# Optimization experiments

Hardware: AMD Instinct MI355X
Metric: run time of the kernel (lower is better)

## Reference

```python
import jax, jax.numpy as jnp
import numpy as np

# ---- static config ----
B, D, H, W, C = 4, 8, 56, 56, 192
Md, Mh, Mw = 2, 7, 7
Sd, Sh, Sw = 1, 3, 3
NH = 6
HD = C // NH
SCALE = HD ** -0.5
N = Md * Mh * Mw  # 98
NW = (D // Md) * (H // Mh) * (W // Mw)  # 256 windows per batch element


def _rel_pos_index():
    coords = np.stack(np.meshgrid(np.arange(Md), np.arange(Mh), np.arange(Mw), indexing='ij'))
    cf = coords.reshape(3, -1)
    rc = (cf[:, :, None] - cf[:, None, :]).transpose(1, 2, 0)
    rc[..., 0] += Md - 1
    rc[..., 1] += Mh - 1
    rc[..., 2] += Mw - 1
    rc[..., 0] *= (2 * Mh - 1) * (2 * Mw - 1)
    rc[..., 1] *= 2 * Mw - 1
    return rc.sum(-1)  # (N, N) int

REL_IDX = jnp.asarray(_rel_pos_index())


def _build_attn_mask():
    img = np.zeros((D, H, W), dtype=np.float32)
    cnt = 0
    for ds in (slice(0, -Md), slice(-Md, -Sd), slice(-Sd, None)):
        for hs in (slice(0, -Mh), slice(-Mh, -Sh), slice(-Sh, None)):
            for ws in (slice(0, -Mw), slice(-Mw, -Sw), slice(-Sw, None)):
                img[ds, hs, ws] = cnt
                cnt += 1
    mw = img.reshape(D // Md, Md, H // Mh, Mh, W // Mw, Mw)
    mw = mw.transpose(0, 2, 4, 1, 3, 5).reshape(-1, N)  # (NW, N)
    am = mw[:, None, :] - mw[:, :, None]
    return np.where(am != 0, -100.0, 0.0).astype(np.float32)  # (NW, N, N)


def window_partition(x):  # (B, D, H, W, C) -> (B*NW, N, C)
    x = x.reshape(B, D // Md, Md, H // Mh, Mh, W // Mw, Mw, C)
    return x.transpose(0, 1, 3, 5, 2, 4, 6, 7).reshape(-1, N, C)


def window_reverse(w):  # (B*NW, N, C) -> (B, D, H, W, C)
    x = w.reshape(B, D // Md, H // Mh, W // Mw, Md, Mh, Mw, C)
    return x.transpose(0, 1, 4, 2, 5, 3, 6, 7).reshape(B, D, H, W, C)


def layer_norm(x, g, b, eps=1e-5):
    mu = x.mean(-1, keepdims=True)
    var = ((x - mu) ** 2).mean(-1, keepdims=True)
    return (x - mu) * jax.lax.rsqrt(var + eps) * g + b


def setup_inputs() -> dict:
    key = jax.random.key(0)
    ks = jax.random.split(key, 6)
    return {
        'x': jax.random.normal(ks[0], (B, D * H * W, C), jnp.float32),
        'attn_mask': jnp.asarray(_build_attn_mask()),
        'norm1_g': jnp.ones((C,), jnp.float32),
        'norm1_b': jnp.zeros((C,), jnp.float32),
        'qkv_w': jax.random.normal(ks[1], (3 * C, C), jnp.float32) * 0.02,
        'qkv_b': jnp.zeros((3 * C,), jnp.float32),
        'rel_bias': jax.random.normal(ks[2], ((2 * Md - 1) * (2 * Mh - 1) * (2 * Mw - 1), NH), jnp.float32) * 0.02,
        'proj_w': jax.random.normal(ks[3], (C, C), jnp.float32) * 0.02,
        'proj_b': jnp.zeros((C,), jnp.float32),
        'fc1_w': jax.random.normal(ks[4], (C, C), jnp.float32) * 0.02,
        'fc1_b': jnp.zeros((C,), jnp.float32),
    }


def reference(x, attn_mask, norm1_g, norm1_b, qkv_w, qkv_b, rel_bias, proj_w, proj_b, fc1_w, fc1_b):
    shortcut = x
    h = layer_norm(x, norm1_g, norm1_b).reshape(B, D, H, W, C)
    # cyclic shift (dims divisible by window -> no padding needed)
    h = jnp.roll(h, shift=(-Sd, -Sh, -Sw), axis=(1, 2, 3))
    xw = window_partition(h)  # (B*NW, N, C)
    B_ = xw.shape[0]
    qkv = (xw @ qkv_w.T + qkv_b).reshape(B_, N, 3, NH, HD).transpose(2, 0, 3, 1, 4)
    q, k, v = qkv[0], qkv[1], qkv[2]  # (B_, NH, N, HD)
    attn = jnp.einsum('bhnd,bhmd->bhnm', q * SCALE, k)
    bias = rel_bias[REL_IDX.reshape(-1)].reshape(N, N, NH).transpose(2, 0, 1)  # (NH, N, N)
    attn = attn + bias[None]
    # additive shift mask per window
    attn = attn.reshape(B, NW, NH, N, N) + attn_mask[None, :, None]
    attn = jax.nn.softmax(attn.reshape(B_, NH, N, N), axis=-1)
    out = jnp.einsum('bhnm,bhmd->bhnd', attn, v).transpose(0, 2, 1, 3).reshape(B_, N, C)
    out = out @ proj_w.T + proj_b
    h = window_reverse(out)
    h = jnp.roll(h, shift=(Sd, Sh, Sw), axis=(1, 2, 3)).reshape(B, D * H * W, C)
    h = jax.nn.gelu(h @ fc1_w.T + fc1_b, approximate=False)
    return shortcut + h
```

## Files before the change

kernel.cpp:

```cpp
#include <hip/hip_runtime.h>
#include <cstdint>
#include <cstddef>

typedef __bf16 bf16_t;
typedef __bf16 bf16x8 __attribute__((ext_vector_type(8)));
typedef float  f32x4  __attribute__((ext_vector_type(4)));

#define DHW   25088
#define SCALE 0.17677669529663687f

__device__ inline f32x4 mfma16(bf16x8 a, bf16x8 b, f32x4 c) {
  return __builtin_amdgcn_mfma_f32_16x16x32_bf16(a, b, c, 0, 0, 0);
}

__device__ inline size_t wrow_to_grow(int orow) {
  int win = orow / 98, tok = orow % 98;
  int b = win >> 8, wr = win & 255;
  int bd = wr >> 6, bh = (wr >> 3) & 7, bwi = wr & 7;
  int md = tok / 49, mh = (tok / 7) % 7, mw = tok % 7;
  int d = (bd * 2 + md + 1) & 7;
  int h = bh * 7 + mh + 3; if (h >= 56) h -= 56;
  int w = bwi * 7 + mw + 3; if (w >= 56) w -= 56;
  return (size_t)b * DHW + (size_t)((d * 56 + h) * 56 + w);
}

__global__ __launch_bounds__(256) void prep_kernel(
    const float* __restrict__ qkv_w, const float* __restrict__ proj_w,
    const float* __restrict__ fc1_w,
    bf16_t* __restrict__ wq, bf16_t* __restrict__ wp, bf16_t* __restrict__ wf)
{
  int idx = blockIdx.x * 256 + threadIdx.x;
  if (idx < 110592) { wq[idx] = (bf16_t)qkv_w[idx]; return; }
  idx -= 110592;
  if (idx < 36864) { wp[idx] = (bf16_t)proj_w[idx]; return; }
  idx -= 36864;
  if (idx < 36864) { wf[idx] = (bf16_t)fc1_w[idx]; }
}

__global__ __launch_bounds__(256) void prep_bm_kernel(
    const float* __restrict__ rel_bias, const float* __restrict__ mask,
    bf16_t* __restrict__ bmr)
{
  int idx = blockIdx.x * 256 + threadIdx.x;
  int e    = idx & 31;
  int lane = (idx >> 5) & 63;
  int t2   = idx >> 11;
  int mt   = t2 % 7;
  int wh   = t2 / 7;
  int type = wh / 6, h = wh - type * 6;
  int winb = ((type & 4) ? 3 : 0) * 64 + ((type & 2) ? 7 : 0) * 8 + ((type & 1) ? 7 : 0);
  int g = lane >> 4, li = lane & 15;
  int nt2 = e >> 2, v = e & 3;
  int row = mt * 16 + g * 4 + v;
  int col = nt2 * 16 + li;
  float val = -1e30f;
  if (row < 98 && col < 98 && nt2 < 7) {
    int di = row / 49 - col / 49 + 1;
    int hi = (row / 7) % 7 - (col / 7) % 7 + 6;
    int wi = row % 7 - col % 7 + 6;
    int rid = di * 169 + hi * 13 + wi;
    val = mask[winb * 9604 + row * 98 + col] + rel_bias[rid * 6 + h];
  }
  bmr[idx] = (bf16_t)val;
}

__global__ __launch_bounds__(448, 2) void fused_kernel(
    const float* __restrict__ x, const float* __restrict__ gw,
    const float* __restrict__ bw_, const bf16_t* __restrict__ wq,
    const float* __restrict__ qkv_b, const bf16_t* __restrict__ wp,
    const float* __restrict__ proj_b, const bf16_t* __restrict__ wf,
    const float* __restrict__ fc1_b, const bf16_t* __restrict__ bmr,
    float* __restrict__ out)
{
  __shared__ __align__(16) char smem[163392];
  bf16_t* U  = (bf16_t*)smem;
  bf16_t* Qs = (bf16_t*)(smem + 30464);
  bf16_t* Ks = (bf16_t*)(smem + 69664);
  bf16_t* Vt = (bf16_t*)(smem + 108864);
  float*  qb = (float*)(smem + 161088);
  float* gwb = (float*)smem;

  #define BS(r, c)  U[(r) * 200 + (c)]
  #define PSd(r, c) U[(r) * 136 + (c)]
  #define QS(r, c)  Qs[(r) * 200 + (c)]
  #define KS(r, c)  Ks[(r) * 200 + (c)]
  #define VT(d, t)  Vt[(d) * 136 + (t)]

  int win  = blockIdx.x;
  int winb = win & 255;
  int type = (((winb >> 6) == 3) ? 4 : 0) | ((((winb >> 3) & 7) == 7) ? 2 : 0)
           | (((winb & 7) == 7) ? 1 : 0);
  int tid  = threadIdx.x;
  int wid  = tid >> 6, lane = tid & 63;
  int g = lane >> 4, li = lane & 15;

  if (tid < 192) { gwb[tid] = gw[tid]; gwb[192 + tid] = bw_[tid]; }
  for (int c = tid; c < 576; c += 448) qb[c] = qkv_b[c];
  {
    uint4 z = {0u, 0u, 0u, 0u};
    for (int c = tid; c < 768; c += 448) {
      int d = c >> 2, part = c & 3;
      *(uint4*)&VT(d, 96 + part * 8) = z;
    }
  }

  int r = wid * 16 + li;
  float v[48];
  if (r < 98) {
    size_t growr = wrow_to_grow(win * 98 + r);
    const float* xr = x + growr * 192 + g * 8;
    #pragma unroll
    for (int ks = 0; ks < 6; ks++) {
      *(float4*)&v[ks * 8]     = *(const float4*)(xr + ks * 32);
      *(float4*)&v[ks * 8 + 4] = *(const float4*)(xr + ks * 32 + 4);
    }
  } else {
    #pragma unroll
    for (int i = 0; i < 48; i++) v[i] = 0.f;
  }
  float s = 0.f, sq = 0.f;
  #pragma unroll
  for (int i = 0; i < 48; i++) { s += v[i]; sq += v[i] * v[i]; }
  s += __shfl_xor(s, 16, 64); sq += __shfl_xor(sq, 16, 64);
  s += __shfl_xor(s, 32, 64); sq += __shfl_xor(sq, 32, 64);
  float mu   = s * (1.0f / 192.0f);
  float var  = sq * (1.0f / 192.0f) - mu * mu;
  float rstd = rsqrtf(var + 1e-5f);
  __syncthreads();
  bf16x8 afr[6];
  #pragma unroll
  for (int ks = 0; ks < 6; ks++) {
    bf16x8 t;
    #pragma unroll
    for (int j = 0; j < 8; j++) {
      int c = ks * 32 + g * 8 + j;
      t[j] = (r < 98) ? (bf16_t)((v[ks * 8 + j] - mu) * rstd * gwb[c] + gwb[192 + c])
                      : (bf16_t)0.0f;
    }
    afr[ks] = t;
  }

  uint4 st[4];
  #pragma unroll
  for (int i = 0; i < 4; i++) {
    int c = tid + 448 * i;
    if (i < 3 || c < 1536) {
      int rr = c / 24, ck = c % 24;
      st[i] = *(const uint4*)(wq + (size_t)rr * 192 + ck * 8);
    }
  }
  for (int nt = 0; nt < 9; nt++) {
    __syncthreads();
    #pragma unroll
    for (int i = 0; i < 4; i++) {
      int c = tid + 448 * i;
      if (i < 3 || c < 1536) {
        int rr = c / 24, ck = c % 24;
        *(uint4*)&BS(rr, ck * 8) = st[i];
      }
    }
    __syncthreads();
    if (nt < 8) {
      #pragma unroll
      for (int i = 0; i < 4; i++) {
        int c = tid + 448 * i;
        if (i < 3 || c < 1536) {
          int rr = c / 24, ck = c % 24;
          st[i] = *(const uint4*)(wq + (size_t)(nt + 1) * 12288 + (size_t)rr * 192 + ck * 8);
        }
      }
    }
    f32x4 acc[4] = {};
    #pragma unroll
    for (int ks = 0; ks < 6; ks++) {
      bf16x8 a = afr[ks];
      #pragma unroll
      for (int ni = 0; ni < 4; ni++) {
        bf16x8 b = *(const bf16x8*)&BS(ni * 16 + li, ks * 32 + g * 8);
        acc[ni] = mfma16(a, b, acc[ni]);
      }
    }
    #pragma unroll
    for (int ni = 0; ni < 4; ni++)
    #pragma unroll
    for (int vv = 0; vv < 4; vv++) {
      int row = wid * 16 + g * 4 + vv;
      if (row < 98) {
        int col = nt * 64 + ni * 16 + li;
        float val = acc[ni][vv] + qb[col];
        if (nt < 3)      QS(row, col)       = (bf16_t)(val * SCALE);
        else if (nt < 6) KS(row, col - 192) = (bf16_t)val;
        else             VT(col - 384, row) = (bf16_t)val;
      }
    }
  }
  __syncthreads();

  int mt  = wid;
  int rq  = mt * 16 + li;
  int rqc = rq < 98 ? rq : 97;
  for (int h = 0; h < 6; h++) {
    const bf16_t* bmp = bmr + ((((size_t)(type * 6 + h)) * 7 + mt) * 64 + lane) * 32;
    bf16x8 bm0 = *(const bf16x8*)(bmp);
    bf16x8 bm1 = *(const bf16x8*)(bmp + 8);
    bf16x8 bm2 = *(const bf16x8*)(bmp + 16);
    bf16x8 bm3 = *(const bf16x8*)(bmp + 24);
    bf16x8 af = *(const bf16x8*)&QS(rqc, h * 32 + g * 8);
    float logit[7][4];
    #pragma unroll
    for (int nt2 = 0; nt2 < 7; nt2++) {
      int rk = nt2 * 16 + li;
      int rkc = rk < 98 ? rk : 97;
      bf16x8 bfr = *(const bf16x8*)&KS(rkc, h * 32 + g * 8);
      f32x4 z = {};
      f32x4 S = mfma16(af, bfr, z);
      #pragma unroll
      for (int vv = 0; vv < 4; vv++) {
        int e = nt2 * 4 + vv;
        float bmv = (e < 8) ? (float)bm0[e] : (e < 16) ? (float)bm1[e - 8]
                  : (e < 24) ? (float)bm2[e - 16] : (float)bm3[e - 24];
        logit[nt2][vv] = S[vv] + bmv;
      }
    }
    #pragma unroll
    for (int vv = 0; vv < 4; vv++) {
      float mx = logit[0][vv];
      #pragma unroll
      for (int nt2 = 1; nt2 < 7; nt2++) mx = fmaxf(mx, logit[nt2][vv]);
      #pragma unroll
      for (int off = 1; off < 16; off <<= 1) mx = fmaxf(mx, __shfl_xor(mx, off, 64));
      float se = 0.f;
      #pragma unroll
      for (int nt2 = 0; nt2 < 7; nt2++) {
        float p = __expf(logit[nt2][vv] - mx);
        logit[nt2][vv] = p; se += p;
      }
      #pragma unroll
      for (int off = 1; off < 16; off <<= 1) se += __shfl_xor(se, off, 64);
      float inv = 1.0f / se;
      int row = mt * 16 + g * 4 + vv;
      #pragma unroll
      for (int nt2 = 0; nt2 < 7; nt2++)
        PSd(row, nt2 * 16 + li) = (bf16_t)(logit[nt2][vv] * inv);
      PSd(row, 112 + li) = (bf16_t)0.0f;
    }
    f32x4 o0 = {}, o1 = {};
    #pragma unroll
    for (int ks = 0; ks < 4; ks++) {
      int ko = ks * 32 + g * 8;
      bf16x8 pf = *(const bf16x8*)&PSd(mt * 16 + li, ko);
      bf16x8 v0 = *(const bf16x8*)&VT(h * 32 + li, ko);
      bf16x8 v1 = *(const bf16x8*)&VT(h * 32 + 16 + li, ko);
      o0 = mfma16(pf, v0, o0);
      o1 = mfma16(pf, v1, o1);
    }
    #pragma unroll
    for (int vv = 0; vv < 4; vv++) {
      int row = mt * 16 + g * 4 + vv;
      if (row < 98) {
        QS(row, h * 32 + li)      = (bf16_t)o0[vv];
        QS(row, h * 32 + 16 + li) = (bf16_t)o1[vv];
      }
    }
  }

  float* bfb = qb;
  if (tid < 192) bfb[tid] = proj_b[tid];
  bf16x8 a2[6];
  #pragma unroll
  for (int ks = 0; ks < 6; ks++)
    a2[ks] = *(const bf16x8*)&QS(rqc, ks * 32 + g * 8);
  #pragma unroll
  for (int i = 0; i < 4; i++) {
    int c = tid + 448 * i;
    if (i < 3 || c < 1536) {
      int rr = c / 24, ck = c % 24;
      st[i] = *(const uint4*)(wp + (size_t)rr * 192 + ck * 8);
    }
  }
  for (int nt = 0; nt < 3; nt++) {
    __syncthreads();
    #pragma unroll
    for (int i = 0; i < 4; i++) {
      int c = tid + 448 * i;
      if (i < 3 || c < 1536) {
        int rr = c / 24, ck = c % 24;
        *(uint4*)&BS(rr, ck * 8) = st[i];
      }
    }
    __syncthreads();
    if (nt < 2) {
      #pragma unroll
      for (int i = 0; i < 4; i++) {
        int c = tid + 448 * i;
        if (i < 3 || c < 1536) {
          int rr = c / 24, ck = c % 24;
          st[i] = *(const uint4*)(wp + (size_t)(nt + 1) * 12288 + (size_t)rr * 192 + ck * 8);
        }
      }
    }
    f32x4 acc[4] = {};
    #pragma unroll
    for (int ks = 0; ks < 6; ks++) {
      bf16x8 a = a2[ks];
      #pragma unroll
      for (int ni = 0; ni < 4; ni++) {
        bf16x8 b = *(const bf16x8*)&BS(ni * 16 + li, ks * 32 + g * 8);
        acc[ni] = mfma16(a, b, acc[ni]);
      }
    }
    #pragma unroll
    for (int ni = 0; ni < 4; ni++)
    #pragma unroll
    for (int vv = 0; vv < 4; vv++) {
      int row = wid * 16 + g * 4 + vv;
      if (row < 98) {
        int col = nt * 64 + ni * 16 + li;
        KS(row, col) = (bf16_t)(acc[ni][vv] + bfb[col]);
      }
    }
  }

  bf16x8 a3[6];
  #pragma unroll
  for (int ks = 0; ks < 6; ks++)
    a3[ks] = *(const bf16x8*)&KS(rqc, ks * 32 + g * 8);
  #pragma unroll
  for (int i = 0; i < 4; i++) {
    int c = tid + 448 * i;
    if (i < 3 || c < 1536) {
      int rr = c / 24, ck = c % 24;
      st[i] = *(const uint4*)(wf + (size_t)rr * 192 + ck * 8);
    }
  }
  size_t growv[4];
  #pragma unroll
  for (int vv = 0; vv < 4; vv++) {
    int row = wid * 16 + g * 4 + vv;
    growv[vv] = (row < 98) ? wrow_to_grow(win * 98 + row) : (size_t)0;
  }
  for (int nt = 0; nt < 3; nt++) {
    __syncthreads();
    #pragma unroll
    for (int i = 0; i < 4; i++) {
      int c = tid + 448 * i;
      if (i < 3 || c < 1536) {
        int rr = c / 24, ck = c % 24;
        *(uint4*)&BS(rr, ck * 8) = st[i];
      }
    }
    if (nt == 0 && tid < 192) bfb[tid] = fc1_b[tid];
    __syncthreads();
    if (nt < 2) {
      #pragma unroll
      for (int i = 0; i < 4; i++) {
        int c = tid + 448 * i;
        if (i < 3 || c < 1536) {
          int rr = c / 24, ck = c % 24;
          st[i] = *(const uint4*)(wf + (size_t)(nt + 1) * 12288 + (size_t)rr * 192 + ck * 8);
        }
      }
    }
    f32x4 acc[4] = {};
    #pragma unroll
    for (int ks = 0; ks < 6; ks++) {
      bf16x8 a = a3[ks];
      #pragma unroll
      for (int ni = 0; ni < 4; ni++) {
        bf16x8 b = *(const bf16x8*)&BS(ni * 16 + li, ks * 32 + g * 8);
        acc[ni] = mfma16(a, b, acc[ni]);
      }
    }
    #pragma unroll
    for (int vv = 0; vv < 4; vv++) {
      int row = wid * 16 + g * 4 + vv;
      if (row < 98) {
        const float* xr = x + growv[vv] * 192;
        float* op = out + growv[vv] * 192;
        #pragma unroll
        for (int ni = 0; ni < 4; ni++) {
          int col = nt * 64 + ni * 16 + li;
          float val = acc[ni][vv] + bfb[col];
          float ge = 0.5f * val * (1.0f + erff(val * 0.70710678118654752f));
          op[col] = xr[col] + ge;
        }
      }
    }
  }
  #undef BS
  #undef PSd
  #undef QS
  #undef KS
  #undef VT
}

extern "C" void kernel_launch(void* const* d_in, const int* in_sizes, int n_in,
                              void* d_out, int out_size, void* d_ws, size_t ws_size,
                              hipStream_t stream) {
  (void)in_sizes; (void)n_in; (void)out_size; (void)ws_size;
  const float* x         = (const float*)d_in[0];
  const float* attn_mask = (const float*)d_in[1];
  const float* n1g       = (const float*)d_in[2];
  const float* n1b       = (const float*)d_in[3];
  const float* qkv_w     = (const float*)d_in[4];
  const float* qkv_b     = (const float*)d_in[5];
  const float* rel_bias  = (const float*)d_in[6];
  const float* proj_w    = (const float*)d_in[7];
  const float* proj_b    = (const float*)d_in[8];
  const float* fc1_w     = (const float*)d_in[9];
  const float* fc1_b     = (const float*)d_in[10];
  float* out = (float*)d_out;

  char* ws = (char*)d_ws;
  size_t off = 0;
  auto alloc = [&](size_t bytes) -> char* {
    char* p = ws + off;
    off += (bytes + 255) & ~(size_t)255;
    return p;
  };
  bf16_t* wq  = (bf16_t*)alloc(110592 * 2);
  bf16_t* wp  = (bf16_t*)alloc(36864 * 2);
  bf16_t* wf  = (bf16_t*)alloc(36864 * 2);
  bf16_t* bmr = (bf16_t*)alloc((size_t)688128 * 2);

  prep_kernel<<<720, 256, 0, stream>>>(qkv_w, proj_w, fc1_w, wq, wp, wf);
  prep_bm_kernel<<<2688, 256, 0, stream>>>(rel_bias, attn_mask, bmr);
  fused_kernel<<<1024, 448, 0, stream>>>(x, n1g, n1b, wq, qkv_b, wp, proj_b,
                                         wf, fc1_b, bmr, out);
}
```

Baseline: 433.2 us.

## Double block to 896 threads splitting N columns and heads across wave pairs

The fused window kernel now runs 14 waves per block instead of 7. Each pair of waves shares a 16-row M tile and splits the GEMM output columns, and the attention heads, between its two waves. The softmax probabilities are staged through a small per-wave LDS chunk rather than a full 98x128 P buffer, which frees LDS, and the two prep kernels are merged into one launch. The aim is more waves in flight per CU and shorter per-wave serial work, at the cost of extra syncs and of giving up the previous launch_bounds hint of two blocks per CU.

```diff
diff --git a/kernel.cpp b/kernel.cpp
--- a/kernel.cpp
+++ b/kernel.cpp
@@ -24,24 +24,21 @@
   return (size_t)b * DHW + (size_t)((d * 56 + h) * 56 + w);
 }
 
-__global__ __launch_bounds__(256) void prep_kernel(
+__global__ __launch_bounds__(256) void prep_all_kernel(
     const float* __restrict__ qkv_w, const float* __restrict__ proj_w,
-    const float* __restrict__ fc1_w,
-    bf16_t* __restrict__ wq, bf16_t* __restrict__ wp, bf16_t* __restrict__ wf)
+    const float* __restrict__ fc1_w, const float* __restrict__ rel_bias,
+    const float* __restrict__ mask,
+    bf16_t* __restrict__ wq, bf16_t* __restrict__ wp, bf16_t* __restrict__ wf,
+    bf16_t* __restrict__ bmr)
 {
   int idx = blockIdx.x * 256 + threadIdx.x;
   if (idx < 110592) { wq[idx] = (bf16_t)qkv_w[idx]; return; }
   idx -= 110592;
   if (idx < 36864) { wp[idx] = (bf16_t)proj_w[idx]; return; }
   idx -= 36864;
-  if (idx < 36864) { wf[idx] = (bf16_t)fc1_w[idx]; }
-}
-
-__global__ __launch_bounds__(256) void prep_bm_kernel(
-    const float* __restrict__ rel_bias, const float* __restrict__ mask,
-    bf16_t* __restrict__ bmr)
-{
-  int idx = blockIdx.x * 256 + threadIdx.x;
+  if (idx < 36864) { wf[idx] = (bf16_t)fc1_w[idx]; return; }
+  idx -= 36864;
+  if (idx >= 688128) return;
   int e    = idx & 31;
   int lane = (idx >> 5) & 63;
   int t2   = idx >> 11;
@@ -64,7 +61,7 @@
   bmr[idx] = (bf16_t)val;
 }
 
-__global__ __launch_bounds__(448, 2) void fused_kernel(
+__global__ __launch_bounds__(896) void fused_kernel(
     const float* __restrict__ x, const float* __restrict__ gw,
     const float* __restrict__ bw_, const bf16_t* __restrict__ wq,
     const float* __restrict__ qkv_b, const bf16_t* __restrict__ wp,
@@ -72,19 +69,19 @@
     const float* __restrict__ fc1_b, const bf16_t* __restrict__ bmr,
     float* __restrict__ out)
 {
-  __shared__ __align__(16) char smem[163392];
+  __shared__ __align__(16) char smem[158528];
   bf16_t* U  = (bf16_t*)smem;
-  bf16_t* Qs = (bf16_t*)(smem + 30464);
-  bf16_t* Ks = (bf16_t*)(smem + 69664);
-  bf16_t* Vt = (bf16_t*)(smem + 108864);
-  float*  qb = (float*)(smem + 161088);
+  bf16_t* Qs = (bf16_t*)(smem + 25600);
+  bf16_t* Ks = (bf16_t*)(smem + 64800);
+  bf16_t* Vt = (bf16_t*)(smem + 104000);
+  float*  qb = (float*)(smem + 156224);
   float* gwb = (float*)smem;
 
-  #define BS(r, c)  U[(r) * 200 + (c)]
-  #define PSd(r, c) U[(r) * 136 + (c)]
-  #define QS(r, c)  Qs[(r) * 200 + (c)]
-  #define KS(r, c)  Ks[(r) * 200 + (c)]
-  #define VT(d, t)  Vt[(d) * 136 + (t)]
+  #define BS(r, c)     U[(r) * 200 + (c)]
+  #define PSc(w, r, c) U[(w) * 640 + (r) * 40 + (c)]
+  #define QS(r, c)     Qs[(r) * 200 + (c)]
+  #define KS(r, c)     Ks[(r) * 200 + (c)]
+  #define VT(d, t)     Vt[(d) * 136 + (t)]
 
   int win  = blockIdx.x;
   int winb = win & 255;
@@ -92,19 +89,18 @@
            | (((winb & 7) == 7) ? 1 : 0);
   int tid  = threadIdx.x;
   int wid  = tid >> 6, lane = tid & 63;
+  int wn = wid & 1, wm = wid >> 1;
   int g = lane >> 4, li = lane & 15;
 
   if (tid < 192) { gwb[tid] = gw[tid]; gwb[192 + tid] = bw_[tid]; }
-  for (int c = tid; c < 576; c += 448) qb[c] = qkv_b[c];
-  {
+  if (tid < 576) qb[tid] = qkv_b[tid];
+  if (tid < 768) {
     uint4 z = {0u, 0u, 0u, 0u};
-    for (int c = tid; c < 768; c += 448) {
-      int d = c >> 2, part = c & 3;
-      *(uint4*)&VT(d, 96 + part * 8) = z;
-    }
-  }
-
-  int r = wid * 16 + li;
+    int d = tid >> 2, part = tid & 3;
+    *(uint4*)&VT(d, 96 + part * 8) = z;
+  }
+
+  int r = wm * 16 + li;
   float v[48];
   if (r < 98) {
     size_t growr = wrow_to_grow(win * 98 + r);
@@ -140,11 +136,11 @@
     afr[ks] = t;
   }
 
-  uint4 st[4];
-  #pragma unroll
-  for (int i = 0; i < 4; i++) {
-    int c = tid + 448 * i;
-    if (i < 3 || c < 1536) {
+  uint4 st[2];
+  #pragma unroll
+  for (int i = 0; i < 2; i++) {
+    int c = tid + 896 * i;
+    if (c < 1536) {
       int rr = c / 24, ck = c % 24;
       st[i] = *(const uint4*)(wq + (size_t)rr * 192 + ck * 8);
     }
@@ -152,9 +148,9 @@
   for (int nt = 0; nt < 9; nt++) {
     __syncthreads();
     #pragma unroll
-    for (int i = 0; i < 4; i++) {
-      int c = tid + 448 * i;
-      if (i < 3 || c < 1536) {
+    for (int i = 0; i < 2; i++) {
+      int c = tid + 896 * i;
+      if (c < 1536) {
         int rr = c / 24, ck = c % 24;
         *(uint4*)&BS(rr, ck * 8) = st[i];
       }
@@ -162,32 +158,32 @@
     __syncthreads();
     if (nt < 8) {
       #pragma unroll
-      for (int i = 0; i < 4; i++) {
-        int c = tid + 448 * i;
-        if (i < 3 || c < 1536) {
+      for (int i = 0; i < 2; i++) {
+        int c = tid + 896 * i;
+        if (c < 1536) {
           int rr = c / 24, ck = c % 24;
           st[i] = *(const uint4*)(wq + (size_t)(nt + 1) * 12288 + (size_t)rr * 192 + ck * 8);
         }
       }
     }
-    f32x4 acc[4] = {};
+    f32x4 acc[2] = {};
     #pragma unroll
     for (int ks = 0; ks < 6; ks++) {
       bf16x8 a = afr[ks];
       #pragma unroll
-      for (int ni = 0; ni < 4; ni++) {
-        bf16x8 b = *(const bf16x8*)&BS(ni * 16 + li, ks * 32 + g * 8);
-        acc[ni] = mfma16(a, b, acc[ni]);
-      }
-    }
-    #pragma unroll
-    for (int ni = 0; ni < 4; ni++)
+      for (int nl = 0; nl < 2; nl++) {
+        bf16x8 b = *(const bf16x8*)&BS((wn * 2 + nl) * 16 + li, ks * 32 + g * 8);
+        acc[nl] = mfma16(a, b, acc[nl]);
+      }
+    }
+    #pragma unroll
+    for (int nl = 0; nl < 2; nl++)
     #pragma unroll
     for (int vv = 0; vv < 4; vv++) {
-      int row = wid * 16 + g * 4 + vv;
+      int row = wm * 16 + g * 4 + vv;
       if (row < 98) {
-        int col = nt * 64 + ni * 16 + li;
-        float val = acc[ni][vv] + qb[col];
+        int col = nt * 64 + (wn * 2 + nl) * 16 + li;
+        float val = acc[nl][vv] + qb[col];
         if (nt < 3)      QS(row, col)       = (bf16_t)(val * SCALE);
         else if (nt < 6) KS(row, col - 192) = (bf16_t)val;
         else             VT(col - 384, row) = (bf16_t)val;
@@ -196,10 +192,11 @@
   }
   __syncthreads();
 
-  int mt  = wid;
+  int mt  = wm;
   int rq  = mt * 16 + li;
   int rqc = rq < 98 ? rq : 97;
-  for (int h = 0; h < 6; h++) {
+  for (int hh = 0; hh < 3; hh++) {
+    int h = wn * 3 + hh;
     const bf16_t* bmp = bmr + ((((size_t)(type * 6 + h)) * 7 + mt) * 64 + lane) * 32;
     bf16x8 bm0 = *(const bf16x8*)(bmp);
     bf16x8 bm1 = *(const bf16x8*)(bmp + 8);
@@ -238,19 +235,24 @@
       #pragma unroll
       for (int off = 1; off < 16; off <<= 1) se += __shfl_xor(se, off, 64);
       float inv = 1.0f / se;
-      int row = mt * 16 + g * 4 + vv;
-      #pragma unroll
-      for (int nt2 = 0; nt2 < 7; nt2++)
-        PSd(row, nt2 * 16 + li) = (bf16_t)(logit[nt2][vv] * inv);
-      PSd(row, 112 + li) = (bf16_t)0.0f;
+      #pragma unroll
+      for (int nt2 = 0; nt2 < 7; nt2++) logit[nt2][vv] *= inv;
     }
     f32x4 o0 = {}, o1 = {};
     #pragma unroll
-    for (int ks = 0; ks < 4; ks++) {
-      int ko = ks * 32 + g * 8;
-      bf16x8 pf = *(const bf16x8*)&PSd(mt * 16 + li, ko);
-      bf16x8 v0 = *(const bf16x8*)&VT(h * 32 + li, ko);
-      bf16x8 v1 = *(const bf16x8*)&VT(h * 32 + 16 + li, ko);
+    for (int ch = 0; ch < 4; ch++) {
+      #pragma unroll
+      for (int nl = 0; nl < 2; nl++) {
+        int nt2 = ch * 2 + nl;
+        #pragma unroll
+        for (int vv = 0; vv < 4; vv++) {
+          bf16_t pv = (nt2 < 7) ? (bf16_t)logit[nt2][vv] : (bf16_t)0.0f;
+          PSc(wid, g * 4 + vv, nl * 16 + li) = pv;
+        }
+      }
+      bf16x8 pf = *(const bf16x8*)&PSc(wid, li, g * 8);
+      bf16x8 v0 = *(const bf16x8*)&VT(h * 32 + li, ch * 32 + g * 8);
+      bf16x8 v1 = *(const bf16x8*)&VT(h * 32 + 16 + li, ch * 32 + g * 8);
       o0 = mfma16(pf, v0, o0);
       o1 = mfma16(pf, v1, o1);
     }
@@ -263,6 +265,7 @@
       }
     }
   }
+  __syncthreads();
 
   float* bfb = qb;
   if (tid < 192) bfb[tid] = proj_b[tid];
@@ -271,9 +274,9 @@
   for (int ks = 0; ks < 6; ks++)
     a2[ks] = *(const bf16x8*)&QS(rqc, ks * 32 + g * 8);
   #pragma unroll
-  for (int i = 0; i < 4; i++) {
-    int c = tid + 448 * i;
-    if (i < 3 || c < 1536) {
+  for (int i = 0; i < 2; i++) {
+    int c = tid + 896 * i;
+    if (c < 1536) {
       int rr = c / 24, ck = c % 24;
       st[i] = *(const uint4*)(wp + (size_t)rr * 192 + ck * 8);
     }
@@ -281,9 +284,9 @@
   for (int nt = 0; nt < 3; nt++) {
     __syncthreads();
     #pragma unroll
-    for (int i = 0; i < 4; i++) {
-      int c = tid + 448 * i;
-      if (i < 3 || c < 1536) {
+    for (int i = 0; i < 2; i++) {
+      int c = tid + 896 * i;
+      if (c < 1536) {
         int rr = c / 24, ck = c % 24;
         *(uint4*)&BS(rr, ck * 8) = st[i];
       }
@@ -291,44 +294,46 @@
     __syncthreads();
     if (nt < 2) {
       #pragma unroll
-      for (int i = 0; i < 4; i++) {
-        int c = tid + 448 * i;
-        if (i < 3 || c < 1536) {
+      for (int i = 0; i < 2; i++) {
+        int c = tid + 896 * i;
+        if (c < 1536) {
           int rr = c / 24, ck = c % 24;
           st[i] = *(const uint4*)(wp + (size_t)(nt + 1) * 12288 + (size_t)rr * 192 + ck * 8);
         }
       }
     }
-    f32x4 acc[4] = {};
+    f32x4 acc[2] = {};
     #pragma unroll
     for (int ks = 0; ks < 6; ks++) {
       bf16x8 a = a2[ks];
       #pragma unroll
-      for (int ni = 0; ni < 4; ni++) {
-        bf16x8 b = *(const bf16x8*)&BS(ni * 16 + li, ks * 32 + g * 8);
-        acc[ni] = mfma16(a, b, acc[ni]);
-      }
-    }
-    #pragma unroll
-    for (int ni = 0; ni < 4; ni++)
+      for (int nl = 0; nl < 2; nl++) {
+        bf16x8 b = *(const bf16x8*)&BS((wn * 2 + nl) * 16 + li, ks * 32 + g * 8);
+        acc[nl] = mfma16(a, b, acc[nl]);
+      }
+    }
+    #pragma unroll
+    for (int nl = 0; nl < 2; nl++)
     #pragma unroll
     for (int vv = 0; vv < 4; vv++) {
-      int row = wid * 16 + g * 4 + vv;
+      int row = wm * 16 + g * 4 + vv;
       if (row < 98) {
-        int col = nt * 64 + ni * 16 + li;
-        KS(row, col) = (bf16_t)(acc[ni][vv] + bfb[col]);
-      }
-    }
-  }
-
+        int col = nt * 64 + (wn * 2 + nl) * 16 + li;
+        KS(row, col) = (bf16_t)(acc[nl][vv] + bfb[col]);
+      }
+    }
+  }
+  __syncthreads();
+
+  if (tid < 192) bfb[tid] = fc1_b[tid];
   bf16x8 a3[6];
   #pragma unroll
   for (int ks = 0; ks < 6; ks++)
     a3[ks] = *(const bf16x8*)&KS(rqc, ks * 32 + g * 8);
   #pragma unroll
-  for (int i = 0; i < 4; i++) {
-    int c = tid + 448 * i;
-    if (i < 3 || c < 1536) {
+  for (int i = 0; i < 2; i++) {
+    int c = tid + 896 * i;
+    if (c < 1536) {
       int rr = c / 24, ck = c % 24;
       st[i] = *(const uint4*)(wf + (size_t)rr * 192 + ck * 8);
     }
@@ -336,51 +341,50 @@
   size_t growv[4];
   #pragma unroll
   for (int vv = 0; vv < 4; vv++) {
-    int row = wid * 16 + g * 4 + vv;
+    int row = wm * 16 + g * 4 + vv;
     growv[vv] = (row < 98) ? wrow_to_grow(win * 98 + row) : (size_t)0;
   }
   for (int nt = 0; nt < 3; nt++) {
     __syncthreads();
     #pragma unroll
-    for (int i = 0; i < 4; i++) {
-      int c = tid + 448 * i;
-      if (i < 3 || c < 1536) {
+    for (int i = 0; i < 2; i++) {
+      int c = tid + 896 * i;
+      if (c < 1536) {
         int rr = c / 24, ck = c % 24;
         *(uint4*)&BS(rr, ck * 8) = st[i];
       }
     }
-    if (nt == 0 && tid < 192) bfb[tid] = fc1_b[tid];
     __syncthreads();
     if (nt < 2) {
       #pragma unroll
-      for (int i = 0; i < 4; i++) {
-        int c = tid + 448 * i;
-        if (i < 3 || c < 1536) {
+      for (int i = 0; i < 2; i++) {
+        int c = tid + 896 * i;
+        if (c < 1536) {
           int rr = c / 24, ck = c % 24;
           st[i] = *(const uint4*)(wf + (size_t)(nt + 1) * 12288 + (size_t)rr * 192 + ck * 8);
         }
       }
     }
-    f32x4 acc[4] = {};
+    f32x4 acc[2] = {};
     #pragma unroll
     for (int ks = 0; ks < 6; ks++) {
       bf16x8 a = a3[ks];
       #pragma unroll
-      for (int ni = 0; ni < 4; ni++) {
-        bf16x8 b = *(const bf16x8*)&BS(ni * 16 + li, ks * 32 + g * 8);
-        acc[ni] = mfma16(a, b, acc[ni]);
+      for (int nl = 0; nl < 2; nl++) {
+        bf16x8 b = *(const bf16x8*)&BS((wn * 2 + nl) * 16 + li, ks * 32 + g * 8);
+        acc[nl] = mfma16(a, b, acc[nl]);
       }
     }
     #pragma unroll
     for (int vv = 0; vv < 4; vv++) {
-      int row = wid * 16 + g * 4 + vv;
+      int row = wm * 16 + g * 4 + vv;
       if (row < 98) {
         const float* xr = x + growv[vv] * 192;
         float* op = out + growv[vv] * 192;
         #pragma unroll
-        for (int ni = 0; ni < 4; ni++) {
-          int col = nt * 64 + ni * 16 + li;
-          float val = acc[ni][vv] + bfb[col];
+        for (int nl = 0; nl < 2; nl++) {
+          int col = nt * 64 + (wn * 2 + nl) * 16 + li;
+          float val = acc[nl][vv] + bfb[col];
           float ge = 0.5f * val * (1.0f + erff(val * 0.70710678118654752f));
           op[col] = xr[col] + ge;
         }
@@ -388,7 +392,7 @@
     }
   }
   #undef BS
-  #undef PSd
+  #undef PSc
   #undef QS
   #undef KS
   #undef VT
@@ -423,8 +427,8 @@
   bf16_t* wf  = (bf16_t*)alloc(36864 * 2);
   bf16_t* bmr = (bf16_t*)alloc((size_t)688128 * 2);
 
-  prep_kernel<<<720, 256, 0, stream>>>(qkv_w, proj_w, fc1_w, wq, wp, wf);
-  prep_bm_kernel<<<2688, 256, 0, stream>>>(rel_bias, attn_mask, bmr);
-  fused_kernel<<<1024, 448, 0, stream>>>(x, n1g, n1b, wq, qkv_b, wp, proj_b,
+  prep_all_kernel<<<3408, 256, 0, stream>>>(qkv_w, proj_w, fc1_w, rel_bias,
+                                            attn_mask, wq, wp, wf, bmr);
+  fused_kernel<<<1024, 896, 0, stream>>>(x, n1g, n1b, wq, qkv_b, wp, proj_b,
                                          wf, fc1_b, bmr, out);
 }
```

Result: faster. 387.0 us (-10.7%).
